# Performance work log

Hardware: AMD Instinct MI355X
Metric: run time of the kernel (lower is better)

The kernel has to match this reference:

```python
import jax, jax.numpy as jnp
import numpy as np

NUM_GROUPS = 32
EPS = 1e-6
NUM_HEADS = 8


def group_norm32(x, gamma, beta):
    # GroupNorm32: compute in float32, cast back to input dtype.
    b, c, h, w = x.shape
    xf = x.astype(jnp.float32).reshape(b, NUM_GROUPS, -1)  # [b, G, (C/G)*h*w]
    mean = xf.mean(axis=-1, keepdims=True)
    var = xf.var(axis=-1, keepdims=True)
    xn = ((xf - mean) * jax.lax.rsqrt(var + EPS)).reshape(b, c, h, w)
    xn = xn * gamma[None, :, None, None] + beta[None, :, None, None]
    return xn.astype(x.dtype)


def setup_inputs() -> dict:
    key = jax.random.key(0)
    ks = jax.random.split(key, 4)
    b, c, h, w = 16, 512, 32, 32
    x = jax.random.normal(ks[0], (b, c, h, w), dtype=jnp.float32)
    w_qkv = jax.random.normal(ks[1], (3 * c, c), dtype=jnp.float32) * (1.0 / np.sqrt(c))
    b_qkv = jnp.zeros((3 * c,), dtype=jnp.float32)
    w_proj = jax.random.normal(ks[2], (c, c), dtype=jnp.float32) * (1.0 / np.sqrt(c))
    b_proj = jnp.zeros((c,), dtype=jnp.float32)
    gamma = jnp.ones((c,), dtype=jnp.float32)
    beta = jnp.zeros((c,), dtype=jnp.float32)
    return {"x": x, "w_qkv": w_qkv, "b_qkv": b_qkv, "w_proj": w_proj,
            "b_proj": b_proj, "gamma": gamma, "beta": beta}


def reference(x, w_qkv, b_qkv, w_proj, b_proj, gamma, beta):
    b, c, h, w = x.shape
    H = NUM_HEADS
    d = c // H
    n = h * w
    x_norm = group_norm32(x, gamma, beta)
    # 1x1 conv == channel matmul
    qkv = jnp.einsum('oc,bchw->bohw', w_qkv, x_norm) + b_qkv[None, :, None, None]
    q, k, v = jnp.split(qkv, 3, axis=1)
    q = q.reshape(b, H, d, n)
    k = k.reshape(b, H, d, n)
    v = v.reshape(b, H, d, n)
    scale = d ** (-0.5)
    attn = jnp.einsum('bhdn,bhdm->bhnm', q, k) * scale  # [b,H,n,n]
    attn = jax.nn.softmax(attn, axis=-1)
    out = jnp.einsum('bhnm,bhdm->bhdn', attn, v).reshape(b, c, h, w)
    proj = jnp.einsum('oc,bchw->bohw', w_proj, out) + b_proj[None, :, None, None]
    return x + proj
```

## Files before the change

### kernel.cpp

```cpp
#include <hip/hip_runtime.h>
#include <hip/hip_bf16.h>

typedef __bf16 bf16;
typedef __bf16 bf16x4 __attribute__((ext_vector_type(4)));
typedef __bf16 bf16x8 __attribute__((ext_vector_type(8)));
typedef float  floatx4 __attribute__((ext_vector_type(4)));

#define BB   16
#define CC   512
#define NN   1024
#define GG   32
#define CPG  16
#define HH   8
#define DD   64
#define QSCALE 0.18033688011f

__device__ inline floatx4 mfma16(bf16x8 a, bf16x8 b, floatx4 c) {
    return __builtin_amdgcn_mfma_f32_16x16x32_bf16(a, b, c, 0, 0, 0);
}

__device__ inline floatx4 zero4() {
    floatx4 z; z[0] = 0.f; z[1] = 0.f; z[2] = 0.f; z[3] = 0.f; return z;
}

__device__ inline void gl_lds16(const bf16* g, bf16* l) {
    __builtin_amdgcn_global_load_lds(
        (const __attribute__((address_space(1))) unsigned int*)g,
        (__attribute__((address_space(3))) unsigned int*)l, 16, 0, 0);
}

__device__ inline float ldf(const void* p, size_t i, int isb) {
    return isb ? (float)((const bf16*)p)[i] : ((const float*)p)[i];
}
__device__ inline floatx4 ldf4(const void* p, size_t i, int isb) {
    floatx4 o;
    if (isb) {
        bf16x4 v = *(const bf16x4*)((const bf16*)p + i);
        #pragma unroll
        for (int j = 0; j < 4; ++j) o[j] = (float)v[j];
    } else {
        o = *(const floatx4*)((const float*)p + i);
    }
    return o;
}
__device__ inline void stf(void* p, size_t i, float v, int isb) {
    if (isb) ((bf16*)p)[i] = (bf16)v; else ((float*)p)[i] = v;
}

__global__ __launch_bounds__(256) void flag_kernel(const void* x, const void* wq,
        const void* wp, const void* gamma, int* flags) {
    __shared__ int bad[3];
    const int tid = threadIdx.x;
    if (tid < 3) bad[tid] = 0;
    __syncthreads();
    const void* arrs[3] = {x, wq, wp};
    #pragma unroll
    for (int a = 0; a < 3; ++a) {
        const unsigned short* u = (const unsigned short*)arrs[a];
        int c = 0;
        for (int i = tid * 32; i < tid * 32 + 32; ++i) {
            if ((u[i] & 0x7F80) == 0x7F80) c = 1;
        }
        if (c) atomicOr(&bad[a], 1);
    }
    __syncthreads();
    if (tid == 0) {
        flags[0] = bad[0] ? 0 : 1;
        flags[1] = bad[1] ? 0 : 1;
        flags[2] = bad[2] ? 0 : 1;
        flags[3] = (((const unsigned short*)gamma)[0] == 0x3F80) ? 1 : 0;
    }
}

__global__ __launch_bounds__(256) void cvt_kernel(const void* __restrict__ src,
        bf16* __restrict__ dst, int n, const int* __restrict__ flags, int fidx) {
    const int f = flags[fidx];
    int i = (blockIdx.x * 256 + threadIdx.x) * 4;
    if (i >= n) return;
    if (f) {
        *(bf16x4*)(dst + i) = *(const bf16x4*)((const bf16*)src + i);
    } else {
        const float* s = (const float*)src + i;
        bf16x4 o;
        #pragma unroll
        for (int j = 0; j < 4; ++j) o[j] = (bf16)s[j];
        *(bf16x4*)(dst + i) = o;
    }
}

__global__ __launch_bounds__(256) void gn_kernel(const void* __restrict__ x,
        const void* __restrict__ gamma, const void* __restrict__ beta,
        bf16* __restrict__ xn_t, const int* __restrict__ flags, int b0) {
    const int fx = flags[0], fg = flags[3];
    const int bg = blockIdx.x;
    const int bl = bg >> 5, g = bg & 31;
    const int tid = threadIdx.x;
    const size_t xbase = (size_t)((b0 + bl) * CC + g * CPG) * NN;

    float s = 0.f, ss = 0.f;
    for (int i = tid * 4; i < CPG * NN; i += 1024) {
        floatx4 v = ldf4(x, xbase + i, fx);
        #pragma unroll
        for (int j = 0; j < 4; ++j) { s += v[j]; ss += v[j] * v[j]; }
    }
    for (int off = 32; off > 0; off >>= 1) {
        s  += __shfl_down(s, off);
        ss += __shfl_down(ss, off);
    }
    __shared__ float red[8];
    __shared__ float stats[2];
    const int wave = tid >> 6;
    if ((tid & 63) == 0) { red[wave] = s; red[4 + wave] = ss; }
    __syncthreads();
    if (tid == 0) {
        float S  = red[0] + red[1] + red[2] + red[3];
        float SS = red[4] + red[5] + red[6] + red[7];
        float mean = S * (1.0f / (CPG * NN));
        float var  = SS * (1.0f / (CPG * NN)) - mean * mean;
        stats[0] = mean;
        stats[1] = rsqrtf(fmaxf(var, 0.f) + 1e-6f);
    }
    __syncthreads();
    const float mean = stats[0], rstd = stats[1];

    __shared__ __align__(16) float tile[CPG][64];
    const int cn = tid >> 4;
    const int nb = (tid & 15) * 4;
    const float gm1 = ldf(gamma, g * CPG + cn, fg);
    const float bt1 = ldf(beta,  g * CPG + cn, fg);
    const int n2 = tid >> 2, cq = tid & 3;
    for (int nt = 0; nt < NN / 64; ++nt) {
        floatx4 v = ldf4(x, xbase + (size_t)cn * NN + nt * 64 + nb, fx);
        #pragma unroll
        for (int j = 0; j < 4; ++j)
            tile[cn][nb + j] = (v[j] - mean) * rstd * gm1 + bt1;
        __syncthreads();
        bf16x4 o;
        #pragma unroll
        for (int k = 0; k < 4; ++k) o[k] = (bf16)tile[cq * 4 + k][n2];
        *(bf16x4*)(xn_t + (size_t)(bl * NN + nt * 64 + n2) * CC + g * CPG + cq * 4) = o;
        __syncthreads();
    }
}

__global__ __launch_bounds__(256) void qkv_kernel(const bf16* __restrict__ wq_b,
        const bf16* __restrict__ b_qkv, const bf16* __restrict__ xn_t,
        bf16* __restrict__ q_t, bf16* __restrict__ k_t, bf16* __restrict__ v_m) {
    __shared__ __align__(16) bf16 As[128 * 32];
    __shared__ __align__(16) bf16 Bs[128 * 32];

    const int ntile = blockIdx.x;
    const int mtile = blockIdx.y;
    const int bl = blockIdx.z;
    const int w = threadIdx.x >> 6, lane = threadIdx.x & 63;
    const int l16 = lane & 15, quad = lane >> 4;
    const int wr = w >> 1, wc = w & 1;

    const int mbase = mtile * 128, nbase = ntile * 128;
    const int srow = lane >> 2, scol = (lane & 3) * 8;
    const bf16* Ag = wq_b + (size_t)(mbase + w * 32 + srow) * CC + scol;
    const bf16* Bg = xn_t + (size_t)bl * NN * CC + (size_t)(nbase + w * 32 + srow) * CC + scol;
    bf16* Al = As + (2 * w) * 512;
    bf16* Bl = Bs + (2 * w) * 512;

    floatx4 acc[4][4];
    #pragma unroll
    for (int i = 0; i < 4; ++i)
        #pragma unroll
        for (int j = 0; j < 4; ++j) acc[i][j] = zero4();

    for (int k0 = 0; k0 < CC; k0 += 32) {
        __syncthreads();
        gl_lds16(Ag + k0, Al);
        gl_lds16(Ag + 16 * CC + k0, Al + 512);
        gl_lds16(Bg + k0, Bl);
        gl_lds16(Bg + 16 * CC + k0, Bl + 512);
        __syncthreads();

        bf16x8 af[4], bfr[4];
        #pragma unroll
        for (int mt = 0; mt < 4; ++mt)
            af[mt] = *(const bf16x8*)&As[(wr * 64 + mt * 16 + l16) * 32 + quad * 8];
        #pragma unroll
        for (int nt = 0; nt < 4; ++nt)
            bfr[nt] = *(const bf16x8*)&Bs[(wc * 64 + nt * 16 + l16) * 32 + quad * 8];
        #pragma unroll
        for (int mt = 0; mt < 4; ++mt)
            #pragma unroll
            for (int nt = 0; nt < 4; ++nt)
                acc[mt][nt] = mfma16(af[mt], bfr[nt], acc[mt][nt]);
    }

    const int qsel = mtile >> 2;
    const int obase = (mtile & 3) * 128;
    #pragma unroll
    for (int mt = 0; mt < 4; ++mt) {
        const int op = obase + wr * 64 + mt * 16 + quad * 4;
        float bias[4];
        #pragma unroll
        for (int r = 0; r < 4; ++r) bias[r] = (float)b_qkv[qsel * CC + op + r];
        #pragma unroll
        for (int nt = 0; nt < 4; ++nt) {
            const int p = nbase + wc * 64 + nt * 16 + l16;
            if (qsel == 0) {
                int h = op >> 6, d0 = op & 63;
                bf16x4 o;
                #pragma unroll
                for (int r = 0; r < 4; ++r) o[r] = (bf16)((acc[mt][nt][r] + bias[r]) * QSCALE);
                *(bf16x4*)(q_t + ((size_t)(bl * HH + h) * NN + p) * DD + d0) = o;
            } else if (qsel == 1) {
                int h = op >> 6, d0 = op & 63;
                bf16x4 o;
                #pragma unroll
                for (int r = 0; r < 4; ++r) o[r] = (bf16)(acc[mt][nt][r] + bias[r]);
                *(bf16x4*)(k_t + ((size_t)(bl * HH + h) * NN + p) * DD + d0) = o;
            } else {
                #pragma unroll
                for (int r = 0; r < 4; ++r)
                    v_m[((size_t)bl * CC + op + r) * NN + p] = (bf16)(acc[mt][nt][r] + bias[r]);
            }
        }
    }
}

__global__ __launch_bounds__(256) void attn_kernel(const bf16* __restrict__ q_t,
        const bf16* __restrict__ k_t, const bf16* __restrict__ v_m,
        bf16* __restrict__ attn_out) {
    const int bh = blockIdx.x;
    const int qt = blockIdx.y;
    const int bl = bh >> 3, h = bh & 7;
    const int tid = threadIdx.x;
    const int wave = tid >> 6, lane = tid & 63;
    const int l16 = lane & 15, quad = lane >> 4;

    __shared__ __align__(16) bf16 Kt[64][72];
    __shared__ __align__(16) bf16 Vt[64][72];
    __shared__ __align__(16) bf16 Pl[4][16][72];

    const bf16* kb = k_t + (size_t)bh * NN * DD;
    const bf16* vb = v_m + (size_t)bh * DD * NN;

    const int r0 = tid >> 3,          c0 = (tid & 7) * 8;
    const int r1 = (tid + 256) >> 3,  c1 = (tid & 7) * 8;
    const bf16* kg0 = kb + (size_t)r0 * DD + c0;
    const bf16* kg1 = kb + (size_t)r1 * DD + c1;
    const bf16* vg0 = vb + (size_t)r0 * NN + c0;
    const bf16* vg1 = vb + (size_t)r1 * NN + c1;

    const int qrow = qt * 64 + wave * 16 + l16;
    const bf16* qp = q_t + ((size_t)bh * NN + qrow) * DD + quad * 8;
    bf16x8 aq0 = *(const bf16x8*)(qp);
    bf16x8 aq1 = *(const bf16x8*)(qp + 32);

    floatx4 oacc[4];
    #pragma unroll
    for (int i = 0; i < 4; ++i) oacc[i] = zero4();
    float lrun = 0.f;

    bf16x8 kr0 = *(const bf16x8*)(kg0);
    bf16x8 kr1 = *(const bf16x8*)(kg1);
    bf16x8 vr0 = *(const bf16x8*)(vg0);
    bf16x8 vr1 = *(const bf16x8*)(vg1);

    for (int m0 = 0; m0 < NN; m0 += 64) {
        __syncthreads();
        *(bf16x8*)&Kt[r0][c0] = kr0;
        *(bf16x8*)&Kt[r1][c1] = kr1;
        *(bf16x8*)&Vt[r0][c0] = vr0;
        *(bf16x8*)&Vt[r1][c1] = vr1;
        if (m0 + 64 < NN) {
            kr0 = *(const bf16x8*)(kg0 + (size_t)(m0 + 64) * DD);
            kr1 = *(const bf16x8*)(kg1 + (size_t)(m0 + 64) * DD);
            vr0 = *(const bf16x8*)(vg0 + m0 + 64);
            vr1 = *(const bf16x8*)(vg1 + m0 + 64);
        }
        __syncthreads();

        floatx4 sacc[4];
        #pragma unroll
        for (int ms = 0; ms < 4; ++ms) {
            sacc[ms] = zero4();
            bf16x8 kf0 = *(const bf16x8*)&Kt[ms * 16 + l16][quad * 8];
            bf16x8 kf1 = *(const bf16x8*)&Kt[ms * 16 + l16][32 + quad * 8];
            sacc[ms] = mfma16(kf0, aq0, sacc[ms]);
            sacc[ms] = mfma16(kf1, aq1, sacc[ms]);
        }

        #pragma unroll
        for (int ms = 0; ms < 4; ++ms) {
            bf16x4 pr;
            #pragma unroll
            for (int r = 0; r < 4; ++r) {
                float p = exp2f(sacc[ms][r]);
                lrun += p;
                pr[r] = (bf16)p;
            }
            *(bf16x4*)&Pl[wave][l16][ms * 16 + quad * 4] = pr;
        }

        #pragma unroll
        for (int ks = 0; ks < 2; ++ks) {
            bf16x8 ap = *(const bf16x8*)&Pl[wave][l16][ks * 32 + quad * 8];
            #pragma unroll
            for (int nt = 0; nt < 4; ++nt) {
                bf16x8 bv = *(const bf16x8*)&Vt[nt * 16 + l16][ks * 32 + quad * 8];
                oacc[nt] = mfma16(ap, bv, oacc[nt]);
            }
        }
    }

    lrun += __shfl_xor(lrun, 16);
    lrun += __shfl_xor(lrun, 32);
    float inv = 1.0f / lrun;
    float ir[4];
    #pragma unroll
    for (int r = 0; r < 4; ++r) ir[r] = __shfl(inv, quad * 4 + r);
    const int p0 = qt * 64 + wave * 16 + quad * 4;
    #pragma unroll
    for (int nt = 0; nt < 4; ++nt) {
        const int c = h * DD + nt * 16 + l16;
        #pragma unroll
        for (int r = 0; r < 4; ++r)
            attn_out[((size_t)bl * NN + p0 + r) * CC + c] = (bf16)(oacc[nt][r] * ir[r]);
    }
}

__global__ __launch_bounds__(256) void proj_kernel(const bf16* __restrict__ wp_b,
        const bf16* __restrict__ b_proj, const bf16* __restrict__ attn_out,
        const void* __restrict__ x, void* __restrict__ out,
        const int* __restrict__ flags, int b0) {
    __shared__ __align__(16) bf16 As[128 * 32];
    __shared__ __align__(16) bf16 Bs[128 * 32];

    const int fx = flags[0];
    const int ntile = blockIdx.x;
    const int mtile = blockIdx.y;
    const int bl = blockIdx.z;
    const int w = threadIdx.x >> 6, lane = threadIdx.x & 63;
    const int l16 = lane & 15, quad = lane >> 4;
    const int wr = w >> 1, wc = w & 1;

    const int mbase = mtile * 128, nbase = ntile * 128;
    const int srow = lane >> 2, scol = (lane & 3) * 8;
    const bf16* Ag = wp_b + (size_t)(mbase + w * 32 + srow) * CC + scol;
    const bf16* Bg = attn_out + (size_t)bl * NN * CC + (size_t)(nbase + w * 32 + srow) * CC + scol;
    bf16* Al = As + (2 * w) * 512;
    bf16* Bl = Bs + (2 * w) * 512;

    floatx4 acc[4][4];
    #pragma unroll
    for (int i = 0; i < 4; ++i)
        #pragma unroll
        for (int j = 0; j < 4; ++j) acc[i][j] = zero4();

    for (int k0 = 0; k0 < CC; k0 += 32) {
        __syncthreads();
        gl_lds16(Ag + k0, Al);
        gl_lds16(Ag + 16 * CC + k0, Al + 512);
        gl_lds16(Bg + k0, Bl);
        gl_lds16(Bg + 16 * CC + k0, Bl + 512);
        __syncthreads();

        bf16x8 af[4], bfr[4];
        #pragma unroll
        for (int mt = 0; mt < 4; ++mt)
            af[mt] = *(const bf16x8*)&As[(wr * 64 + mt * 16 + l16) * 32 + quad * 8];
        #pragma unroll
        for (int nt = 0; nt < 4; ++nt)
            bfr[nt] = *(const bf16x8*)&Bs[(wc * 64 + nt * 16 + l16) * 32 + quad * 8];
        #pragma unroll
        for (int mt = 0; mt < 4; ++mt)
            #pragma unroll
            for (int nt = 0; nt < 4; ++nt)
                acc[mt][nt] = mfma16(af[mt], bfr[nt], acc[mt][nt]);
    }

    #pragma unroll
    for (int mt = 0; mt < 4; ++mt) {
        const int op = mbase + wr * 64 + mt * 16 + quad * 4;
        float bias[4];
        #pragma unroll
        for (int r = 0; r < 4; ++r) bias[r] = (float)b_proj[op + r];
        #pragma unroll
        for (int nt = 0; nt < 4; ++nt) {
            const int p = nbase + wc * 64 + nt * 16 + l16;
            #pragma unroll
            for (int r = 0; r < 4; ++r) {
                size_t idx = ((size_t)(b0 + bl) * CC + op + r) * NN + p;
                float xv = ldf(x, idx, fx);
                stf(out, idx, xv + acc[mt][nt][r] + bias[r], fx);
            }
        }
    }
}

extern "C" void kernel_launch(void* const* d_in, const int* in_sizes, int n_in,
                              void* d_out, int out_size, void* d_ws, size_t ws_size,
                              hipStream_t stream) {
    const void* x      = d_in[0];
    const void* w_qkv  = d_in[1];
    const bf16* b_qkv  = (const bf16*)d_in[2];
    const void* w_proj = d_in[3];
    const bf16* b_proj = (const bf16*)d_in[4];
    const void* gamma  = d_in[5];
    const void* beta   = d_in[6];

    const size_t MB = (size_t)1 << 20;
    const int NQKV = 3 * CC * CC;
    const int NPRJ = CC * CC;
    const size_t wbytes = (size_t)(NQKV + NPRJ) * sizeof(bf16) + 4096;
    int bc = 0;
    for (int c = 16; c >= 1; c >>= 1) {
        if ((size_t)c * 4 * MB + wbytes <= ws_size) { bc = c; break; }
    }
    if (bc == 0) {
        hipMemsetAsync(d_out, 0, (size_t)out_size * sizeof(bf16), stream);
        return;
    }

    const size_t cs = (size_t)bc * MB;
    char* ws = (char*)d_ws;
    bf16* xn_t = (bf16*)(ws);
    bf16* q_t  = (bf16*)(ws + cs);
    bf16* k_t  = (bf16*)(ws + 2 * cs);
    bf16* v_m  = (bf16*)(ws + 3 * cs);
    int*  flags = (int*)(ws + 4 * cs);
    bf16* wq_b = (bf16*)(ws + 4 * cs + 4096);
    bf16* wp_b = wq_b + NQKV;
    bf16* attn_out = xn_t;

    flag_kernel<<<1, 256, 0, stream>>>(x, w_qkv, w_proj, gamma, flags);
    cvt_kernel<<<NQKV / 1024, 256, 0, stream>>>(w_qkv, wq_b, NQKV, flags, 1);
    cvt_kernel<<<NPRJ / 1024, 256, 0, stream>>>(w_proj, wp_b, NPRJ, flags, 2);

    for (int b0 = 0; b0 < BB; b0 += bc) {
        gn_kernel<<<dim3(bc * GG), 256, 0, stream>>>(x, gamma, beta, xn_t, flags, b0);
        qkv_kernel<<<dim3(8, 12, bc), 256, 0, stream>>>(wq_b, b_qkv, xn_t, q_t, k_t, v_m);
        attn_kernel<<<dim3(bc * HH, 16), 256, 0, stream>>>(q_t, k_t, v_m, attn_out);
        proj_kernel<<<dim3(8, 4, bc), 256, 0, stream>>>(wp_b, b_proj, attn_out, x, d_out, flags, b0);
    }
}
```

Before: 259.8 us.

## Rewrite attention with 32x32 MFMA, register-resident P, and double-buffered async K/V loads

The attention kernel moves from 16x16x32 to 32x32x16 bf16 MFMA tiles, so each wave handles 32 query rows and each block 128. The softmax probabilities are packed to bf16 and rearranged across lanes with permlane32 swaps, so they feed the PV matmul from registers instead of round-tripping through LDS. K/V tiles are loaded with global_load_lds into swizzled, double-buffered shared memory, overlapping the next tile's fetch with the current tile's compute, and exp2 uses the hardware intrinsic. The aims are fewer LDS round-trips, fewer MFMA instructions and hidden global-load latency, at the cost of higher register pressure and a fragile lane-layout and swizzle scheme.

```diff
diff --git a/kernel.cpp b/kernel.cpp
--- a/kernel.cpp
+++ b/kernel.cpp
@@ -5,6 +5,7 @@
 typedef __bf16 bf16x4 __attribute__((ext_vector_type(4)));
 typedef __bf16 bf16x8 __attribute__((ext_vector_type(8)));
 typedef float  floatx4 __attribute__((ext_vector_type(4)));
+typedef float  f32x16  __attribute__((ext_vector_type(16)));
 
 #define BB   16
 #define CC   512
@@ -15,8 +16,17 @@
 #define DD   64
 #define QSCALE 0.18033688011f
 
+#if __has_builtin(__builtin_amdgcn_exp2f)
+#define EXP2(x) __builtin_amdgcn_exp2f(x)
+#else
+#define EXP2(x) exp2f(x)
+#endif
+
 __device__ inline floatx4 mfma16(bf16x8 a, bf16x8 b, floatx4 c) {
     return __builtin_amdgcn_mfma_f32_16x16x32_bf16(a, b, c, 0, 0, 0);
+}
+__device__ inline f32x16 mfma32(bf16x8 a, bf16x8 b, f32x16 c) {
+    return __builtin_amdgcn_mfma_f32_32x32x16_bf16(a, b, c, 0, 0, 0);
 }
 
 __device__ inline floatx4 zero4() {
@@ -27,6 +37,15 @@
     __builtin_amdgcn_global_load_lds(
         (const __attribute__((address_space(1))) unsigned int*)g,
         (__attribute__((address_space(3))) unsigned int*)l, 16, 0, 0);
+}
+
+__device__ inline unsigned cvt_pk_bf16(float a, float b) {
+    unsigned r;
+    asm("v_cvt_pk_bf16_f32 %0, %1, %2" : "=v"(r) : "v"(a), "v"(b));
+    return r;
+}
+__device__ inline void pl32swap(unsigned &x, unsigned &y) {
+    asm volatile("v_permlane32_swap_b32 %0, %1" : "+v"(x), "+v"(y));
 }
 
 __device__ inline float ldf(const void* p, size_t i, int isb) {
@@ -226,102 +245,110 @@
 __global__ __launch_bounds__(256) void attn_kernel(const bf16* __restrict__ q_t,
         const bf16* __restrict__ k_t, const bf16* __restrict__ v_m,
         bf16* __restrict__ attn_out) {
-    const int bh = blockIdx.x;
-    const int qt = blockIdx.y;
+    const int qb = blockIdx.x;
+    const int bh = blockIdx.y;
     const int bl = bh >> 3, h = bh & 7;
     const int tid = threadIdx.x;
-    const int wave = tid >> 6, lane = tid & 63;
-    const int l16 = lane & 15, quad = lane >> 4;
-
-    __shared__ __align__(16) bf16 Kt[64][72];
-    __shared__ __align__(16) bf16 Vt[64][72];
-    __shared__ __align__(16) bf16 Pl[4][16][72];
+    const int w = tid >> 6, lane = tid & 63;
+    const int l31 = lane & 31, hi = lane >> 5;
+
+    __shared__ __align__(16) bf16 Kt[2][64 * 64];
+    __shared__ __align__(16) bf16 Vt[2][64 * 64];
 
     const bf16* kb = k_t + (size_t)bh * NN * DD;
     const bf16* vb = v_m + (size_t)bh * DD * NN;
 
-    const int r0 = tid >> 3,          c0 = (tid & 7) * 8;
-    const int r1 = (tid + 256) >> 3,  c1 = (tid & 7) * 8;
-    const bf16* kg0 = kb + (size_t)r0 * DD + c0;
-    const bf16* kg1 = kb + (size_t)r1 * DD + c1;
-    const bf16* vg0 = vb + (size_t)r0 * NN + c0;
-    const bf16* vg1 = vb + (size_t)r1 * NN + c1;
-
-    const int qrow = qt * 64 + wave * 16 + l16;
-    const bf16* qp = q_t + ((size_t)bh * NN + qrow) * DD + quad * 8;
-    bf16x8 aq0 = *(const bf16x8*)(qp);
-    bf16x8 aq1 = *(const bf16x8*)(qp + 32);
-
-    floatx4 oacc[4];
-    #pragma unroll
-    for (int i = 0; i < 4; ++i) oacc[i] = zero4();
+    const int r8 = lane >> 3, sl = lane & 7;
+    const int gcol = ((sl ^ r8) << 3);
+    const int w16 = w * 16;
+
+#define STAGE(buf, m0) do {                                                       \
+    gl_lds16(kb + (size_t)((m0) + w16 + r8) * DD + gcol,     &Kt[buf][(w16) * 64]);     \
+    gl_lds16(kb + (size_t)((m0) + w16 + 8 + r8) * DD + gcol, &Kt[buf][(w16 + 8) * 64]); \
+    gl_lds16(vb + (size_t)(w16 + r8) * NN + (m0) + gcol,     &Vt[buf][(w16) * 64]);     \
+    gl_lds16(vb + (size_t)(w16 + 8 + r8) * NN + (m0) + gcol, &Vt[buf][(w16 + 8) * 64]); \
+} while (0)
+
+    const int qrow = qb * 128 + w * 32 + l31;
+    const bf16* qp = q_t + ((size_t)bh * NN + qrow) * DD + hi * 8;
+    bf16x8 qf[4];
+    #pragma unroll
+    for (int ks = 0; ks < 4; ++ks) qf[ks] = *(const bf16x8*)(qp + ks * 16);
+
+    f32x16 oacc[2];
+    #pragma unroll
+    for (int i = 0; i < 2; ++i)
+        #pragma unroll
+        for (int r = 0; r < 16; ++r) oacc[i][r] = 0.f;
     float lrun = 0.f;
 
-    bf16x8 kr0 = *(const bf16x8*)(kg0);
-    bf16x8 kr1 = *(const bf16x8*)(kg1);
-    bf16x8 vr0 = *(const bf16x8*)(vg0);
-    bf16x8 vr1 = *(const bf16x8*)(vg1);
-
-    for (int m0 = 0; m0 < NN; m0 += 64) {
-        __syncthreads();
-        *(bf16x8*)&Kt[r0][c0] = kr0;
-        *(bf16x8*)&Kt[r1][c1] = kr1;
-        *(bf16x8*)&Vt[r0][c0] = vr0;
-        *(bf16x8*)&Vt[r1][c1] = vr1;
-        if (m0 + 64 < NN) {
-            kr0 = *(const bf16x8*)(kg0 + (size_t)(m0 + 64) * DD);
-            kr1 = *(const bf16x8*)(kg1 + (size_t)(m0 + 64) * DD);
-            vr0 = *(const bf16x8*)(vg0 + m0 + 64);
-            vr1 = *(const bf16x8*)(vg1 + m0 + 64);
-        }
-        __syncthreads();
-
-        floatx4 sacc[4];
-        #pragma unroll
-        for (int ms = 0; ms < 4; ++ms) {
-            sacc[ms] = zero4();
-            bf16x8 kf0 = *(const bf16x8*)&Kt[ms * 16 + l16][quad * 8];
-            bf16x8 kf1 = *(const bf16x8*)&Kt[ms * 16 + l16][32 + quad * 8];
-            sacc[ms] = mfma16(kf0, aq0, sacc[ms]);
-            sacc[ms] = mfma16(kf1, aq1, sacc[ms]);
-        }
-
-        #pragma unroll
-        for (int ms = 0; ms < 4; ++ms) {
-            bf16x4 pr;
-            #pragma unroll
-            for (int r = 0; r < 4; ++r) {
-                float p = exp2f(sacc[ms][r]);
-                lrun += p;
-                pr[r] = (bf16)p;
+    STAGE(0, 0);
+
+    for (int it = 0; it < 16; ++it) {
+        const int cur = it & 1;
+        const int nm0 = ((it + 1) & 15) * 64;
+        STAGE(cur ^ 1, nm0);
+        asm volatile("s_waitcnt vmcnt(4)" ::: "memory");
+        __builtin_amdgcn_s_barrier();
+        asm volatile("" ::: "memory");
+
+        const bf16* KtB = Kt[cur];
+        const bf16* VtB = Vt[cur];
+
+        #pragma unroll
+        for (int kb2 = 0; kb2 < 2; ++kb2) {
+            const int krow = kb2 * 32 + l31;
+            const int ksw = krow & 7;
+            f32x16 s;
+            #pragma unroll
+            for (int r = 0; r < 16; ++r) s[r] = 0.f;
+            #pragma unroll
+            for (int ks = 0; ks < 4; ++ks) {
+                bf16x8 kf = *(const bf16x8*)(KtB + krow * 64 + (((2 * ks + hi) ^ ksw) << 3));
+                s = mfma32(kf, qf[ks], s);
             }
-            *(bf16x4*)&Pl[wave][l16][ms * 16 + quad * 4] = pr;
-        }
-
-        #pragma unroll
-        for (int ks = 0; ks < 2; ++ks) {
-            bf16x8 ap = *(const bf16x8*)&Pl[wave][l16][ks * 32 + quad * 8];
-            #pragma unroll
-            for (int nt = 0; nt < 4; ++nt) {
-                bf16x8 bv = *(const bf16x8*)&Vt[nt * 16 + l16][ks * 32 + quad * 8];
-                oacc[nt] = mfma16(ap, bv, oacc[nt]);
+            float p[16];
+            #pragma unroll
+            for (int r = 0; r < 16; ++r) { p[r] = EXP2(s[r]); lrun += p[r]; }
+            unsigned pw[8];
+            #pragma unroll
+            for (int i = 0; i < 8; ++i) pw[i] = cvt_pk_bf16(p[2 * i], p[2 * i + 1]);
+            pl32swap(pw[0], pw[2]); pl32swap(pw[1], pw[3]);
+            pl32swap(pw[4], pw[6]); pl32swap(pw[5], pw[7]);
+
+            #pragma unroll
+            for (int tt = 0; tt < 2; ++tt) {
+                union { unsigned u[4]; bf16x8 v; } pf;
+                pf.u[0] = pw[tt * 4 + 0]; pf.u[1] = pw[tt * 4 + 1];
+                pf.u[2] = pw[tt * 4 + 2]; pf.u[3] = pw[tt * 4 + 3];
+                const int t = kb2 * 2 + tt;
+                #pragma unroll
+                for (int db = 0; db < 2; ++db) {
+                    const int vrow = db * 32 + l31;
+                    bf16x8 vf = *(const bf16x8*)(VtB + vrow * 64 +
+                                                 (((2 * t + hi) ^ (vrow & 7)) << 3));
+                    oacc[db] = mfma32(vf, pf.v, oacc[db]);
+                }
             }
         }
-    }
-
-    lrun += __shfl_xor(lrun, 16);
+        asm volatile("s_waitcnt lgkmcnt(0)" ::: "memory");
+        __builtin_amdgcn_s_barrier();
+        asm volatile("" ::: "memory");
+    }
+#undef STAGE
+
     lrun += __shfl_xor(lrun, 32);
-    float inv = 1.0f / lrun;
-    float ir[4];
-    #pragma unroll
-    for (int r = 0; r < 4; ++r) ir[r] = __shfl(inv, quad * 4 + r);
-    const int p0 = qt * 64 + wave * 16 + quad * 4;
-    #pragma unroll
-    for (int nt = 0; nt < 4; ++nt) {
-        const int c = h * DD + nt * 16 + l16;
-        #pragma unroll
-        for (int r = 0; r < 4; ++r)
-            attn_out[((size_t)bl * NN + p0 + r) * CC + c] = (bf16)(oacc[nt][r] * ir[r]);
+    const float inv = 1.0f / lrun;
+    bf16* ob = attn_out + ((size_t)bl * NN + qrow) * CC + h * DD;
+    #pragma unroll
+    for (int db = 0; db < 2; ++db) {
+        #pragma unroll
+        for (int g = 0; g < 4; ++g) {
+            bf16x4 o;
+            #pragma unroll
+            for (int e = 0; e < 4; ++e) o[e] = (bf16)(oacc[db][4 * g + e] * inv);
+            *(bf16x4*)(ob + db * 32 + g * 8 + hi * 4) = o;
+        }
     }
 }
 
@@ -436,7 +463,7 @@
     for (int b0 = 0; b0 < BB; b0 += bc) {
         gn_kernel<<<dim3(bc * GG), 256, 0, stream>>>(x, gamma, beta, xn_t, flags, b0);
         qkv_kernel<<<dim3(8, 12, bc), 256, 0, stream>>>(wq_b, b_qkv, xn_t, q_t, k_t, v_m);
-        attn_kernel<<<dim3(bc * HH, 16), 256, 0, stream>>>(q_t, k_t, v_m, attn_out);
+        attn_kernel<<<dim3(8, bc * HH), 256, 0, stream>>>(q_t, k_t, v_m, attn_out);
         proj_kernel<<<dim3(8, 4, bc), 256, 0, stream>>>(wp_b, b_proj, attn_out, x, d_out, flags, b0);
     }
 }
```

New measurement: 245.8 us. 5.4% less time.
